# Kernel tuning notes

Hardware: AMD Instinct MI355X
Metric: run time of the kernel (lower is better)

The kernel has to match this reference:

```python
import jax, jax.numpy as jnp
import numpy as np
from functools import partial

REG = 0.1
NUM_ITERS = 50
EPS_NORM = 1e-8
EPS_SINK = 1e-10


def _cdist(x0, x1):
    # torch.cdist(p=2): pairwise euclidean distance [B,N,N]
    sq0 = jnp.sum(x0 * x0, axis=-1)                     # [B,N]
    sq1 = jnp.sum(x1 * x1, axis=-1)                     # [B,N]
    inner = jnp.einsum('bnd,bmd->bnm', x0, x1)          # [B,N,N]
    d2 = sq0[:, :, None] + sq1[:, None, :] - 2.0 * inner
    return jnp.sqrt(jnp.maximum(d2, 0.0))


def setup_inputs() -> dict:
    key = jax.random.key(0)
    k0, k1 = jax.random.split(key)
    B, N, D = 8, 2048, 64
    x0 = jax.random.normal(k0, (B, N, D), dtype=jnp.float32)
    x1 = jax.random.normal(k1, (B, N, D), dtype=jnp.float32)
    return {"x0": x0, "x1": x1}


def reference(x0, x1):
    B, N, D = x0.shape
    # cost matrix + per-batch max normalization
    C = _cdist(x0, x1)
    C = C / (jnp.max(C, axis=(-2, -1), keepdims=True) + EPS_NORM)
    # Gibbs kernel
    K = jnp.exp(-C / REG)                               # [B,N,N]
    # Sinkhorn fixed-point iterations
    u0 = jnp.full((B, N), 1.0 / N, dtype=K.dtype)
    v0 = jnp.full((B, N), 1.0 / N, dtype=K.dtype)

    def body(i, uv):
        u, v = uv
        u = 1.0 / (jnp.einsum('bij,bj->bi', K, v) + EPS_SINK)
        v = 1.0 / (jnp.einsum('bij,bi->bj', K, u) + EPS_SINK)
        return (u, v)

    u, v = jax.lax.fori_loop(0, NUM_ITERS, body, (u0, v0))
    # transport plan P = diag(u) K diag(v)
    P = u[:, :, None] * K * v[:, None, :]               # [B,N,N]
    # greedy matching: argmax over columns
    matchings = jnp.argmax(P, axis=-1)                  # [B,N] int
    return matchings
```

## Files before the change

### kernel.cpp

```cpp
#include <hip/hip_runtime.h>
#include <stdint.h>

#define BB 8
#define NN 2048
#define DD 64
#define REGv 0.1f
#define NUM_ITERS 50
#define EPS_NORM 1e-8f
#define EPS_SINK 1e-10f

typedef float f4 __attribute__((ext_vector_type(4)));
typedef __attribute__((address_space(1))) const void GV;
typedef __attribute__((address_space(3))) void LV;

__device__ __forceinline__ float dotf4(f4 a, f4 b) {
    return a.x * b.x + a.y * b.y + a.z * b.z + a.w * b.w;
}

__global__ void init_k(unsigned* maxd, unsigned* bar) {
    int t = blockIdx.x * 256 + threadIdx.x;
    if (t < BB) maxd[t] = 0u;
    if (t < NUM_ITERS * 8 * 32) bar[t] = 0u;
}

__global__ void sq_k(const float* __restrict__ x0, const float* __restrict__ x1,
                     float* __restrict__ sq0, float* __restrict__ sq1) {
    int w = (blockIdx.x * 256 + threadIdx.x) >> 6;
    int lane = threadIdx.x & 63;
    if (w >= 2 * BB * NN) return;
    const float* src = (w < BB * NN) ? x0 : x1;
    int r = (w < BB * NN) ? w : w - BB * NN;
    float val = src[(size_t)r * DD + lane];
    float s = val * val;
    #pragma unroll
    for (int off = 32; off; off >>= 1) s += __shfl_xor(s, off);
    if (lane == 0) ((w < BB * NN) ? sq0 : sq1)[r] = s;
}

template<int WRITE>
__global__ __launch_bounds__(256) void distc_k(const float* __restrict__ x0,
                                               const float* __restrict__ x1,
                                               const float* __restrict__ sq0,
                                               const float* __restrict__ sq1,
                                               float* __restrict__ Kd,
                                               unsigned* __restrict__ maxd) {
    __shared__ float x0s[128 * 64];
    __shared__ float x1t[64 * 68];
    __shared__ float wred[4];
    int bid = blockIdx.x;
    int b = bid >> 9;
    int tile = bid & 511;
    int ti = tile >> 5, tj = tile & 31;
    int i0 = ti * 128, j0 = tj * 64;
    int t = threadIdx.x;

    const float4* g0 = (const float4*)(x0 + ((size_t)b * NN + i0) * DD);
    #pragma unroll
    for (int rep = 0; rep < 8; rep++) {
        int e = rep * 256 + t;
        int row = e >> 4, c4 = e & 15;
        int pc = c4 ^ ((row >> 3) & 3);
        *(float4*)&x0s[row * 64 + pc * 4] = g0[row * 16 + c4];
    }
    const float4* g1 = (const float4*)(x1 + ((size_t)b * NN + j0) * DD);
    #pragma unroll
    for (int rep = 0; rep < 4; rep++) {
        int e = rep * 256 + t;
        int row = e >> 4, c4 = e & 15;
        float4 a = g1[row * 16 + c4];
        x1t[(c4 * 4 + 0) * 68 + row] = a.x;
        x1t[(c4 * 4 + 1) * 68 + row] = a.y;
        x1t[(c4 * 4 + 2) * 68 + row] = a.z;
        x1t[(c4 * 4 + 3) * 68 + row] = a.w;
    }
    __syncthreads();

    int tx = t & 15, ty = t >> 4;
    float4 acc4[8];
    #pragma unroll
    for (int di = 0; di < 8; di++) acc4[di] = make_float4(0.f, 0.f, 0.f, 0.f);

    #pragma unroll
    for (int k4 = 0; k4 < 16; k4++) {
        float4 b0 = *(const float4*)&x1t[(k4 * 4 + 0) * 68 + tx * 4];
        float4 b1 = *(const float4*)&x1t[(k4 * 4 + 1) * 68 + tx * 4];
        float4 b2 = *(const float4*)&x1t[(k4 * 4 + 2) * 68 + tx * 4];
        float4 b3 = *(const float4*)&x1t[(k4 * 4 + 3) * 68 + tx * 4];
        int pk = (k4 ^ (ty & 3)) << 2;
        #pragma unroll
        for (int di = 0; di < 8; di++) {
            float4 a = *(const float4*)&x0s[(ty * 8 + di) * 64 + pk];
            acc4[di].x += a.x * b0.x + a.y * b1.x + a.z * b2.x + a.w * b3.x;
            acc4[di].y += a.x * b0.y + a.y * b1.y + a.z * b2.y + a.w * b3.y;
            acc4[di].z += a.x * b0.z + a.y * b1.z + a.z * b2.z + a.w * b3.z;
            acc4[di].w += a.x * b0.w + a.y * b1.w + a.z * b2.w + a.w * b3.w;
        }
    }

    int ib = b * NN + i0 + ty * 8;
    float4 s1 = *(const float4*)&sq1[b * NN + j0 + tx * 4];

    if (WRITE) {
        float mv = sqrtf(__uint_as_float(maxd[b])) + EPS_NORM;
        #pragma unroll
        for (int di = 0; di < 8; di++) {
            float s0 = sq0[ib + di];
            float4 o;
            o.x = expf(-((sqrtf(fmaxf(s0 + s1.x - 2.f * acc4[di].x, 0.f)) / mv) / REGv));
            o.y = expf(-((sqrtf(fmaxf(s0 + s1.y - 2.f * acc4[di].y, 0.f)) / mv) / REGv));
            o.z = expf(-((sqrtf(fmaxf(s0 + s1.z - 2.f * acc4[di].z, 0.f)) / mv) / REGv));
            o.w = expf(-((sqrtf(fmaxf(s0 + s1.w - 2.f * acc4[di].w, 0.f)) / mv) / REGv));
            *(float4*)&Kd[(size_t)(ib + di) * NN + j0 + tx * 4] = o;
        }
    } else {
        float lm = 0.0f;
        #pragma unroll
        for (int di = 0; di < 8; di++) {
            float s0 = sq0[ib + di];
            lm = fmaxf(lm, fmaxf(s0 + s1.x - 2.f * acc4[di].x, 0.f));
            lm = fmaxf(lm, fmaxf(s0 + s1.y - 2.f * acc4[di].y, 0.f));
            lm = fmaxf(lm, fmaxf(s0 + s1.z - 2.f * acc4[di].z, 0.f));
            lm = fmaxf(lm, fmaxf(s0 + s1.w - 2.f * acc4[di].w, 0.f));
        }
        #pragma unroll
        for (int off = 32; off; off >>= 1) lm = fmaxf(lm, __shfl_xor(lm, off));
        if ((t & 63) == 0) wred[t >> 6] = lm;
        __syncthreads();
        if (t == 0) {
            float m = fmaxf(fmaxf(wred[0], wred[1]), fmaxf(wred[2], wred[3]));
            atomicMax(&maxd[b], __float_as_uint(m));
        }
    }
}

__device__ __forceinline__ void gbar(unsigned* c, int t, unsigned n) {
    __syncthreads();
    if (t == 0) {
        __threadfence();
        atomicAdd(c, 1u);
        while (__hip_atomic_load(c, __ATOMIC_RELAXED, __HIP_MEMORY_SCOPE_AGENT) < n)
            __builtin_amdgcn_s_sleep(2);
        __threadfence();
    }
    __syncthreads();
}

__global__ __launch_bounds__(512)
void persist_k(const float* __restrict__ Kd,
               float* __restrict__ partial,
               float* __restrict__ vglob,
               float* __restrict__ uglob,
               unsigned* __restrict__ bar) {
    __shared__ f4 S[2][8][512];
    __shared__ f4 vbuf4[512];
    __shared__ f4 sgbuf[512];

    const int t = threadIdx.x;
    const int l = t & 63;
    const int w = t >> 6;
    const int q = blockIdx.x;
    const int b = q & 7;
    const int g = q >> 3;
    const size_t rowbase = (size_t)b * NN + (size_t)g * 64;

    vbuf4[t] = (f4){1.0f / NN, 1.0f / NN, 1.0f / NN, 1.0f / NN};
    __syncthreads();

#define STAGE(c_) do { \
    const float* rp_ = Kd + (rowbase + (size_t)(c_) * 8 + (size_t)w) * NN; \
    char* lb_ = (char*)(&S[(c_) & 1][w][0]); \
    _Pragma("unroll") \
    for (int j_ = 0; j_ < 8; ++j_) { \
        __builtin_amdgcn_global_load_lds((GV*)(rp_ + (j_ * 64 + l) * 4), \
                                         (LV*)(lb_ + j_ * 1024), 16, 0, 0); \
    } } while (0)

    STAGE(0); STAGE(1);

    int db = 0;
    for (int it = 0; it < NUM_ITERS; ++it) {
        const bool last = (it == NUM_ITERS - 1);
        f4 sg[8];
        #pragma unroll
        for (int k = 0; k < 8; ++k) sg[k] = (f4){0.f, 0.f, 0.f, 0.f};

        for (int c = 0; c < 8; ++c) {
            if (c < 7) asm volatile("s_waitcnt vmcnt(8)" ::: "memory");
            else       asm volatile("s_waitcnt vmcnt(0)" ::: "memory");
            __builtin_amdgcn_sched_barrier(0);

            f4 kk[8];
            #pragma unroll
            for (int k = 0; k < 8; ++k) kk[k] = S[c & 1][w][(((w + k) & 7) << 6) + l];
            float dp = 0.f;
            #pragma unroll
            for (int k = 0; k < 8; ++k) dp += dotf4(kk[k], vbuf4[(((w + k) & 7) << 6) + l]);
            #pragma unroll
            for (int off = 32; off; off >>= 1) dp += __shfl_xor(dp, off);
            float uu = 1.0f / (dp + EPS_SINK);
            if (last && l == 0) uglob[rowbase + (size_t)c * 8 + w] = uu;
            #pragma unroll
            for (int k = 0; k < 8; ++k) sg[k] += uu * kk[k];

            if (c < 6) {
                asm volatile("s_waitcnt lgkmcnt(0)" ::: "memory");
                __builtin_amdgcn_sched_barrier(0);
                STAGE(c + 2);
            }
        }

        #pragma unroll
        for (int s = 0; s < 8; ++s) {
            int idx = (((w + s) & 7) << 6) + l;
            if (s == 0) sgbuf[idx] = sg[0];
            else        sgbuf[idx] += sg[s];
            __syncthreads();
        }

        ((f4*)partial)[(size_t)((db * 8 + b) * 32 + g) * 512 + t] = sgbuf[t];
        gbar(bar + ((size_t)it * 8 + b) * 32, t, 32u);

        f4 vs = (f4){0.f, 0.f, 0.f, 0.f};
        const f4* pp = (const f4*)partial + (size_t)(db * 8 + b) * 32 * 512 + t;
        #pragma unroll
        for (int gg = 0; gg < 32; ++gg) vs += pp[gg * 512];
        f4 vv;
        vv.x = 1.0f / (vs.x + EPS_SINK);
        vv.y = 1.0f / (vs.y + EPS_SINK);
        vv.z = 1.0f / (vs.z + EPS_SINK);
        vv.w = 1.0f / (vs.w + EPS_SINK);
        if (last && g == 0) ((f4*)vglob)[b * 512 + t] = vv;
        vbuf4[t] = vv;
        __syncthreads();
        db ^= 1;
        if (!last) { STAGE(0); STAGE(1); }
    }
#undef STAGE
}

__global__ __launch_bounds__(256) void argmax_k(const float* __restrict__ Kd,
                                                const float* __restrict__ u,
                                                const float* __restrict__ v,
                                                int* __restrict__ out) {
    int w = (blockIdx.x * 256 + threadIdx.x) >> 6;
    int lane = threadIdx.x & 63;
    int b = w >> 11, i = w & 2047;
    float uu = u[(size_t)b * NN + i];
    const float4* Kr = (const float4*)(Kd + ((size_t)b * NN + i) * NN);
    const float4* v4 = (const float4*)(v + (size_t)b * NN);
    float best = -1.0f;
    int bidx = 0;
    for (int it = 0; it < 8; it++) {
        int c4 = it * 64 + lane;
        float4 kk = Kr[c4];
        float4 vv = v4[c4];
        int j = c4 * 4;
        float p0 = (uu * kk.x) * vv.x;
        float p1 = (uu * kk.y) * vv.y;
        float p2 = (uu * kk.z) * vv.z;
        float p3 = (uu * kk.w) * vv.w;
        if (p0 > best) { best = p0; bidx = j; }
        if (p1 > best) { best = p1; bidx = j + 1; }
        if (p2 > best) { best = p2; bidx = j + 2; }
        if (p3 > best) { best = p3; bidx = j + 3; }
    }
    #pragma unroll
    for (int off = 32; off; off >>= 1) {
        float ov = __shfl_xor(best, off);
        int oi = __shfl_xor(bidx, off);
        if (ov > best || (ov == best && oi < bidx)) { best = ov; bidx = oi; }
    }
    if (lane == 0) out[(size_t)b * NN + i] = bidx;
}

extern "C" void kernel_launch(void* const* d_in, const int* in_sizes, int n_in,
                              void* d_out, int out_size, void* d_ws, size_t ws_size,
                              hipStream_t stream) {
    const float* x0 = (const float*)d_in[0];
    const float* x1 = (const float*)d_in[1];
    int* out = (int*)d_out;
    char* ws = (char*)d_ws;

    float* Kd      = (float*)(ws + 0ull);
    float* partial = (float*)(ws + 134217728ull);
    float* vglob   = (float*)(ws + 138412032ull);
    float* uglob   = (float*)(ws + 138477568ull);
    float* sq0     = (float*)(ws + 138543104ull);
    float* sq1     = (float*)(ws + 138608640ull);
    unsigned* maxd = (unsigned*)(ws + 138674176ull);
    unsigned* bar  = (unsigned*)(ws + 138674304ull);

    init_k<<<50, 256, 0, stream>>>(maxd, bar);
    sq_k<<<8192, 256, 0, stream>>>(x0, x1, sq0, sq1);
    distc_k<0><<<4096, 256, 0, stream>>>(x0, x1, sq0, sq1, Kd, maxd);
    distc_k<1><<<4096, 256, 0, stream>>>(x0, x1, sq0, sq1, Kd, maxd);
    persist_k<<<256, 512, 0, stream>>>(Kd, partial, vglob, uglob, bar);
    argmax_k<<<4096, 256, 0, stream>>>(Kd, uglob, vglob, out);
}
```

Before: 1.751 ms.

## Distribute column reduction across blocks with second barrier and cross-iteration prefetch

After: 2.553 ms. 1.46x slower.

```diff
diff --git a/kernel.cpp b/kernel.cpp
--- a/kernel.cpp
+++ b/kernel.cpp
@@ -20,7 +20,7 @@
 __global__ void init_k(unsigned* maxd, unsigned* bar) {
     int t = blockIdx.x * 256 + threadIdx.x;
     if (t < BB) maxd[t] = 0u;
-    if (t < NUM_ITERS * 8 * 32) bar[t] = 0u;
+    if (t < 2 * NUM_ITERS * 8 * 32) bar[t] = 0u;
 }
 
 __global__ void sq_k(const float* __restrict__ x0, const float* __restrict__ x1,
@@ -159,8 +159,8 @@
     const int l = t & 63;
     const int w = t >> 6;
     const int q = blockIdx.x;
-    const int b = q & 7;
-    const int g = q >> 3;
+    const int b = q >> 5;
+    const int g = q & 31;
     const size_t rowbase = (size_t)b * NN + (size_t)g * 64;
 
     vbuf4[t] = (f4){1.0f / NN, 1.0f / NN, 1.0f / NN, 1.0f / NN};
@@ -177,7 +177,6 @@
 
     STAGE(0); STAGE(1);
 
-    int db = 0;
     for (int it = 0; it < NUM_ITERS; ++it) {
         const bool last = (it == NUM_ITERS - 1);
         f4 sg[8];
@@ -185,8 +184,8 @@
         for (int k = 0; k < 8; ++k) sg[k] = (f4){0.f, 0.f, 0.f, 0.f};
 
         for (int c = 0; c < 8; ++c) {
-            if (c < 7) asm volatile("s_waitcnt vmcnt(8)" ::: "memory");
-            else       asm volatile("s_waitcnt vmcnt(0)" ::: "memory");
+            if (last && c == 7) asm volatile("s_waitcnt vmcnt(0)" ::: "memory");
+            else                asm volatile("s_waitcnt vmcnt(8)" ::: "memory");
             __builtin_amdgcn_sched_barrier(0);
 
             f4 kk[8];
@@ -202,10 +201,10 @@
             #pragma unroll
             for (int k = 0; k < 8; ++k) sg[k] += uu * kk[k];
 
-            if (c < 6) {
+            if (!(last && c >= 6)) {
                 asm volatile("s_waitcnt lgkmcnt(0)" ::: "memory");
                 __builtin_amdgcn_sched_barrier(0);
-                STAGE(c + 2);
+                STAGE((c + 2) & 7);
             }
         }
 
@@ -217,23 +216,38 @@
             __syncthreads();
         }
 
-        ((f4*)partial)[(size_t)((db * 8 + b) * 32 + g) * 512 + t] = sgbuf[t];
+        ((f4*)partial)[(size_t)q * 512 + t] = sgbuf[t];
         gbar(bar + ((size_t)it * 8 + b) * 32, t, 32u);
 
-        f4 vs = (f4){0.f, 0.f, 0.f, 0.f};
-        const f4* pp = (const f4*)partial + (size_t)(db * 8 + b) * 32 * 512 + t;
-        #pragma unroll
-        for (int gg = 0; gg < 32; ++gg) vs += pp[gg * 512];
-        f4 vv;
-        vv.x = 1.0f / (vs.x + EPS_SINK);
-        vv.y = 1.0f / (vs.y + EPS_SINK);
-        vv.z = 1.0f / (vs.z + EPS_SINK);
-        vv.w = 1.0f / (vs.w + EPS_SINK);
-        if (last && g == 0) ((f4*)vglob)[b * 512 + t] = vv;
-        vbuf4[t] = vv;
+        {
+            int c4 = g * 16 + (t & 15);
+            int prow = t >> 4;
+            f4 pv = ((const f4*)partial)[(size_t)(b * 32 + prow) * 512 + c4];
+            #pragma unroll
+            for (int off = 16; off <= 32; off <<= 1) {
+                pv.x += __shfl_xor(pv.x, off);
+                pv.y += __shfl_xor(pv.y, off);
+                pv.z += __shfl_xor(pv.z, off);
+                pv.w += __shfl_xor(pv.w, off);
+            }
+            if (l < 16) sgbuf[w * 16 + l] = pv;
+            __syncthreads();
+            if (t < 16) {
+                f4 s = sgbuf[t];
+                #pragma unroll
+                for (int ww = 1; ww < 8; ww++) s += sgbuf[ww * 16 + t];
+                f4 vv;
+                vv.x = 1.0f / (s.x + EPS_SINK);
+                vv.y = 1.0f / (s.y + EPS_SINK);
+                vv.z = 1.0f / (s.z + EPS_SINK);
+                vv.w = 1.0f / (s.w + EPS_SINK);
+                ((f4*)vglob)[b * 512 + g * 16 + t] = vv;
+            }
+        }
+        gbar(bar + ((size_t)(NUM_ITERS + it) * 8 + b) * 32, t, 32u);
+
+        vbuf4[t] = ((const f4*)vglob)[b * 512 + t];
         __syncthreads();
-        db ^= 1;
-        if (!last) { STAGE(0); STAGE(1); }
     }
 #undef STAGE
 }
@@ -283,14 +297,14 @@
 
     float* Kd      = (float*)(ws + 0ull);
     float* partial = (float*)(ws + 134217728ull);
-    float* vglob   = (float*)(ws + 138412032ull);
-    float* uglob   = (float*)(ws + 138477568ull);
-    float* sq0     = (float*)(ws + 138543104ull);
-    float* sq1     = (float*)(ws + 138608640ull);
-    unsigned* maxd = (unsigned*)(ws + 138674176ull);
-    unsigned* bar  = (unsigned*)(ws + 138674304ull);
-
-    init_k<<<50, 256, 0, stream>>>(maxd, bar);
+    float* vglob   = (float*)(ws + 136314880ull);
+    float* uglob   = (float*)(ws + 136380416ull);
+    float* sq0     = (float*)(ws + 136445952ull);
+    float* sq1     = (float*)(ws + 136511488ull);
+    unsigned* maxd = (unsigned*)(ws + 136577024ull);
+    unsigned* bar  = (unsigned*)(ws + 136577152ull);
+
+    init_k<<<100, 256, 0, stream>>>(maxd, bar);
     sq_k<<<8192, 256, 0, stream>>>(x0, x1, sq0, sq1);
     distc_k<0><<<4096, 256, 0, stream>>>(x0, x1, sq0, sq1, Kd, maxd);
     distc_k<1><<<4096, 256, 0, stream>>>(x0, x1, sq0, sq1, Kd, maxd);
```
